# Optimization experiments

Hardware: AMD Instinct MI355X
Metric: run time of the kernel (lower is better)

## Reference

```python
import jax, jax.numpy as jnp
import numpy as np

EMBED_DIM = 1024
N_HEADS = 16
DK = EMBED_DIM // N_HEADS


def setup_inputs() -> dict:
    key = jax.random.key(0)
    ks = jax.random.split(key, 8)
    B, S, D = 2, 2048, EMBED_DIM
    s = 1.0 / np.sqrt(D)
    return {
        'key': jax.random.normal(ks[0], (B, S, D), jnp.float32),
        'query': jax.random.normal(ks[1], (B, S, D), jnp.float32),
        'value': jax.random.normal(ks[2], (B, S, D), jnp.float32),
        'Wq': jax.random.normal(ks[3], (D, D), jnp.float32) * s,
        'Wk': jax.random.normal(ks[4], (D, D), jnp.float32) * s,
        'Wv': jax.random.normal(ks[5], (D, D), jnp.float32) * s,
        'Wo': jax.random.normal(ks[6], (D, D), jnp.float32) * s,
        'bo': jax.random.normal(ks[7], (D,), jnp.float32) * 0.01,
    }


def reference(key, query, value, Wq, Wk, Wv, Wo, bo):
    # torch nn.Linear computes x @ W.T; weights here are [out, in]
    B, Sk, D = key.shape
    Sq = query.shape[1]
    H, dk = N_HEADS, DK
    # project and split heads: [B, H, S, dk]
    Q = (query @ Wq.T).reshape(B, Sq, H, dk).transpose(0, 2, 1, 3)
    K = (key @ Wk.T).reshape(B, Sk, H, dk).transpose(0, 2, 1, 3)
    V = (value @ Wv.T).reshape(B, Sk, H, dk).transpose(0, 2, 1, 3)
    scores = jnp.einsum('bhqd,bhkd->bhqk', Q, K) / jnp.sqrt(jnp.float32(dk))
    attn = jax.nn.softmax(scores, axis=-1)
    ctx = jnp.einsum('bhqk,bhkd->bhqd', attn, V)  # [B, H, Sq, dk]
    concat = ctx.transpose(0, 2, 1, 3).reshape(B, Sq, H * dk)
    return concat @ Wo.T + bo
```

## Files before the change

kernel.cpp:

```cpp
#include <hip/hip_runtime.h>
#include <hip/hip_bf16.h>
#include <stdint.h>


#define D_MODEL 1024
#define NH      16
#define DKH     64
#define SEQ     2048
#define BATCH   2
#define M_TOT   (BATCH * SEQ)
#define XSZ     (M_TOT * D_MODEL)
#define WSZ     (D_MODEL * D_MODEL)
#define NT      (SEQ / 64)
#define NKT     (D_MODEL / 64)

#define SCALE_Q 0.18033688011112042f
#define SHIFT2  5.770780163555854f

typedef _Float16 f16x8 __attribute__((ext_vector_type(8)));
typedef _Float16 f16x4 __attribute__((ext_vector_type(4)));
typedef __fp16   h16x2 __attribute__((ext_vector_type(2)));
typedef float    f32x4v __attribute__((ext_vector_type(4)));

typedef __attribute__((address_space(1))) const void gas_void;
typedef __attribute__((address_space(3))) void las_void;

__device__ __forceinline__ void gload16(const _Float16* g, _Float16* l) {
    __builtin_amdgcn_global_load_lds((gas_void*)g, (las_void*)l, 16, 0, 0);
}

__device__ __forceinline__ float fast_exp2(float x) {
    return __builtin_amdgcn_exp2f(x);
}

__global__ __launch_bounds__(256)
void cvt_all(const float* __restrict__ xq, const float* __restrict__ xk,
             const float* __restrict__ xv,
             const float* __restrict__ wq, const float* __restrict__ wk,
             const float* __restrict__ wv, const float* __restrict__ wo,
             _Float16* __restrict__ oxq, _Float16* __restrict__ oxk,
             _Float16* __restrict__ oxv,
             _Float16* __restrict__ owq, _Float16* __restrict__ owk,
             _Float16* __restrict__ owv, _Float16* __restrict__ owo) {
    const int z = blockIdx.z;
    if (z >= 3 && blockIdx.x >= WSZ / 1024) return;
    const float* s = z == 0 ? xq : z == 1 ? xk : z == 2 ? xv :
                     z == 3 ? wq : z == 4 ? wk : z == 5 ? wv : wo;
    _Float16*    d = z == 0 ? oxq : z == 1 ? oxk : z == 2 ? oxv :
                     z == 3 ? owq : z == 4 ? owk : z == 5 ? owv : owo;
    float sc = z == 3 ? SCALE_Q : 1.0f;
    int i = blockIdx.x * 256 + threadIdx.x;
    float4 x = ((const float4*)s)[i];
    f16x4 h = {(_Float16)(x.x * sc), (_Float16)(x.y * sc),
               (_Float16)(x.z * sc), (_Float16)(x.w * sc)};
    ((f16x4*)d)[i] = h;
}

__global__ __launch_bounds__(256)
void qkv_proj(const _Float16* __restrict__ Xq, const _Float16* __restrict__ Xk,
              const _Float16* __restrict__ Xv,
              const _Float16* __restrict__ Wq, const _Float16* __restrict__ Wk,
              const _Float16* __restrict__ Wv,
              _Float16* __restrict__ Qo, _Float16* __restrict__ Ko,
              _Float16* __restrict__ Vt) {
    const int which = blockIdx.z;
    const _Float16* X = which == 0 ? Xq : which == 1 ? Xk : Xv;
    const _Float16* W = which == 0 ? Wq : which == 1 ? Wk : Wv;

    __shared__ __align__(16) _Float16 A[2 * 128 * 64];
    __shared__ __align__(16) _Float16 B[2 * 64 * 64];

    const int t = threadIdx.x;
    const int lane = t & 63, wv = t >> 6;
    const int l15 = lane & 15, quad = lane >> 4;
    const int wm = (wv >> 1) * 64, wn = (wv & 1) * 32;
    const int n0 = blockIdx.y * 64, m0 = blockIdx.x * 128;
    const int srow = lane >> 3;
    const int scol = ((lane & 7) ^ srow) * 8;

    const int achunk0 = wv * 4;
    const int arow0 = achunk0 * 8 + srow;
    const int aldsb = achunk0 * 512 + lane * 8;
    const int bchunk0 = wv * 2;
    const int brow0 = bchunk0 * 8 + srow;
    const int bldsb = bchunk0 * 512 + lane * 8;

    f32x4v acc[4][2] = {};

    #pragma unroll
    for (int c = 0; c < 4; ++c)
        gload16(X + (size_t)(m0 + arow0 + c * 8) * D_MODEL + scol,
                &A[aldsb + c * 512]);
    #pragma unroll
    for (int c = 0; c < 2; ++c)
        gload16(W + (size_t)(n0 + brow0 + c * 8) * D_MODEL + scol,
                &B[bldsb + c * 512]);

    for (int kt = 0; kt < NKT; ++kt) {
        const int acb = (kt & 1) * 8192, apb = acb ^ 8192;
        const int bcb = (kt & 1) * 4096, bpb = bcb ^ 4096;

        __builtin_amdgcn_s_barrier();

        if (kt < NKT - 1) {
            const int k0 = (kt + 1) * 64;
            #pragma unroll
            for (int c = 0; c < 4; ++c)
                gload16(X + (size_t)(m0 + arow0 + c * 8) * D_MODEL + k0 + scol,
                        &A[apb + aldsb + c * 512]);
            #pragma unroll
            for (int c = 0; c < 2; ++c)
                gload16(W + (size_t)(n0 + brow0 + c * 8) * D_MODEL + k0 + scol,
                        &B[bpb + bldsb + c * 512]);
            asm volatile("s_waitcnt vmcnt(6)" ::: "memory");
        } else {
            asm volatile("s_waitcnt vmcnt(0)" ::: "memory");
        }
        __builtin_amdgcn_sched_barrier(0);

        #pragma unroll
        for (int ks = 0; ks < 2; ++ks) {
            const int g = ((ks * 4 + quad) ^ (l15 & 7)) * 8;
            f16x8 a[4], b[2];
            #pragma unroll
            for (int mi = 0; mi < 4; ++mi)
                a[mi] = *(const f16x8*)&A[acb + (wm + mi * 16 + l15) * 64 + g];
            #pragma unroll
            for (int ni = 0; ni < 2; ++ni)
                b[ni] = *(const f16x8*)&B[bcb + (wn + ni * 16 + l15) * 64 + g];
            #pragma unroll
            for (int mi = 0; mi < 4; ++mi)
                #pragma unroll
                for (int ni = 0; ni < 2; ++ni)
                    acc[mi][ni] = __builtin_amdgcn_mfma_f32_16x16x32_f16(
                        a[mi], b[ni], acc[mi][ni], 0, 0, 0);
        }
    }

    #pragma unroll
    for (int mi = 0; mi < 4; ++mi)
        #pragma unroll
        for (int r = 0; r < 4; ++r) {
            int m = m0 + wm + mi * 16 + quad * 4 + r;
            int bb = m >> 11, s = m & (SEQ - 1);
            #pragma unroll
            for (int ni = 0; ni < 2; ++ni) {
                int col = n0 + wn + ni * 16 + l15;
                int h = col >> 6, d = col & 63;
                _Float16 v = (_Float16)acc[mi][ni][r];
                if (which == 2)
                    Vt[((size_t)(bb * NH + h) * DKH + d) * SEQ + s] = v;
                else if (which == 0)
                    Qo[((size_t)(bb * NH + h) * SEQ + s) * DKH + d] = v;
                else
                    Ko[((size_t)(bb * NH + h) * SEQ + s) * DKH + d] = v;
            }
        }
}

__global__ __launch_bounds__(512)
void attn_kernel(const _Float16* __restrict__ Qg, const _Float16* __restrict__ Kg,
                 const _Float16* __restrict__ Vtg, _Float16* __restrict__ Cg) {
    __shared__ __align__(16) _Float16 Qs[128 * 64];
    __shared__ __align__(16) _Float16 Ks[2 * 64 * 64];
    __shared__ __align__(16) _Float16 Vs[2 * 64 * 64];
    __shared__ __align__(16) _Float16 PsT[128 * 64];
    const int t = threadIdx.x;
    const int lane = t & 63, wv = t >> 6;
    const int l15 = lane & 15, quad = lane >> 4;
    const int bh = blockIdx.x, q0 = blockIdx.y * 128;
    const _Float16* Qb = Qg + (size_t)bh * SEQ * DKH;
    const _Float16* Kb = Kg + (size_t)bh * SEQ * DKH;
    const _Float16* Vb = Vtg + (size_t)bh * DKH * SEQ;

    const int srow = lane >> 3;
    const int scol = ((lane & 7) ^ srow) * 8;
    const int r7 = l15 & 7;

    const int krow = wv * 8 + srow;
    const int off = wv * 512 + lane * 8;
    const _Float16* kp = Kb + (size_t)krow * DKH + scol;
    const _Float16* vp = Vb + (size_t)krow * SEQ + scol;

    #pragma unroll
    for (int c = 0; c < 2; ++c) {
        int chunk = wv * 2 + c;
        int row = chunk * 8 + srow;
        gload16(Qb + (size_t)(q0 + row) * DKH + scol, &Qs[chunk * 512 + lane * 8]);
    }
    gload16(kp, &Ks[off]);
    gload16(vp, &Vs[off]);
    __syncthreads();

    f16x8 bq[2];
    {
        int row = wv * 16 + l15;
        #pragma unroll
        for (int ks = 0; ks < 2; ++ks)
            bq[ks] = *(const f16x8*)&Qs[row * 64 +
                                        (((ks * 4 + quad) ^ (row & 7)) * 8)];
    }

    f32x4v O[4] = {};
    f32x4v lacc = {};
    const f16x8 ones = {(_Float16)1.0f, (_Float16)1.0f, (_Float16)1.0f,
                        (_Float16)1.0f, (_Float16)1.0f, (_Float16)1.0f,
                        (_Float16)1.0f, (_Float16)1.0f};

    const _Float16* kA = kp + 64 * DKH;
    const _Float16* vA = vp + 64;

    for (int ti = 0; ti < NT; ++ti) {
        const int cb = (ti & 1) * 4096;
        const int pb = cb ^ 4096;

        __builtin_amdgcn_s_barrier();

        if (ti < NT - 1) {
            gload16(kA, &Ks[pb + off]);
            gload16(vA, &Vs[pb + off]);
            kA += 64 * DKH; vA += 64;
            asm volatile("s_waitcnt vmcnt(2)" ::: "memory");
        } else {
            asm volatile("s_waitcnt vmcnt(0)" ::: "memory");
        }
        __builtin_amdgcn_sched_barrier(0);

        f32x4v sf[4];
        #pragma unroll
        for (int c = 0; c < 4; ++c)
            sf[c] = f32x4v{-SHIFT2, -SHIFT2, -SHIFT2, -SHIFT2};

        __builtin_amdgcn_s_setprio(1);
        #pragma unroll
        for (int ks = 0; ks < 2; ++ks) {
            const int g = ((ks * 4 + quad) ^ r7) * 8;
            #pragma unroll
            for (int c = 0; c < 4; ++c) {
                f16x8 ak = *(const f16x8*)&Ks[cb + (c * 16 + l15) * 64 + g];
                sf[c] = __builtin_amdgcn_mfma_f32_16x16x32_f16(
                    ak, bq[ks], sf[c], 0, 0, 0);
            }
        }
        __builtin_amdgcn_s_setprio(0);

        const int prow = wv * 16 + l15;
        #pragma unroll
        for (int c = 0; c < 4; ++c) {
            float p0 = fast_exp2(sf[c][0]);
            float p1 = fast_exp2(sf[c][1]);
            float p2 = fast_exp2(sf[c][2]);
            float p3 = fast_exp2(sf[c][3]);
            union { f16x4 v; h16x2 h[2]; } u;
            u.h[0] = __builtin_amdgcn_cvt_pkrtz(p0, p1);
            u.h[1] = __builtin_amdgcn_cvt_pkrtz(p2, p3);
            const int swzcol = (((2 * c + (quad >> 1)) ^ r7) * 8) +
                               (quad & 1) * 4;
            *(f16x4*)&PsT[prow * 64 + swzcol] = u.v;
        }

        #pragma unroll
        for (int ks = 0; ks < 2; ++ks) {
            const int g = ((ks * 4 + quad) ^ r7) * 8;
            f16x8 bp = *(const f16x8*)&PsT[prow * 64 + g];
            __builtin_amdgcn_s_setprio(1);
            lacc = __builtin_amdgcn_mfma_f32_16x16x32_f16(
                ones, bp, lacc, 0, 0, 0);
            #pragma unroll
            for (int di = 0; di < 4; ++di) {
                f16x8 av = *(const f16x8*)&Vs[cb + (di * 16 + l15) * 64 + g];
                O[di] = __builtin_amdgcn_mfma_f32_16x16x32_f16(
                    av, bp, O[di], 0, 0, 0);
            }
            __builtin_amdgcn_s_setprio(0);
        }
    }

    {
        float inv = 1.0f / lacc[0];
        int q = q0 + wv * 16 + l15;
        _Float16* Crow = Cg + ((size_t)bh * SEQ + q) * DKH;
        #pragma unroll
        for (int di = 0; di < 4; ++di) {
            f16x4 oh = {(_Float16)(O[di][0] * inv), (_Float16)(O[di][1] * inv),
                        (_Float16)(O[di][2] * inv), (_Float16)(O[di][3] * inv)};
            *(f16x4*)&Crow[di * 16 + quad * 4] = oh;
        }
    }
}

__global__ __launch_bounds__(256)
void oproj(const _Float16* __restrict__ Ch, const _Float16* __restrict__ Wo,
           const float* __restrict__ bo, float* __restrict__ out) {
    __shared__ __align__(16) _Float16 A[2 * 64 * 64];
    __shared__ __align__(16) _Float16 B[2 * 128 * 64];
    const int t = threadIdx.x;
    const int lane = t & 63, wv = t >> 6;
    const int l15 = lane & 15, quad = lane >> 4;
    const int wm = (wv >> 1) * 32, wn = (wv & 1) * 64;
    const int n0 = blockIdx.y * 128, m0 = blockIdx.x * 64;
    const int srow = lane >> 3;
    const int scol = ((lane & 7) ^ srow) * 8;
    const int bb = m0 >> 11, sbase = m0 & (SEQ - 1);

    const int achunk0 = wv * 2;
    const int arow0 = achunk0 * 8 + srow;
    const int aldsb = achunk0 * 512 + lane * 8;
    const int bchunk0 = wv * 4;
    const int brow0 = bchunk0 * 8 + srow;
    const int bldsb = bchunk0 * 512 + lane * 8;

    f32x4v acc[2][4] = {};

    #pragma unroll
    for (int c = 0; c < 2; ++c)
        gload16(Ch + ((size_t)(bb * NH + 0) * SEQ + sbase + arow0 + c * 8) * DKH + scol,
                &A[aldsb + c * 512]);
    #pragma unroll
    for (int c = 0; c < 4; ++c)
        gload16(Wo + (size_t)(n0 + brow0 + c * 8) * D_MODEL + scol,
                &B[bldsb + c * 512]);

    for (int kt = 0; kt < NKT; ++kt) {
        const int acb = (kt & 1) * 4096, apb = acb ^ 4096;
        const int bcb = (kt & 1) * 8192, bpb = bcb ^ 8192;

        __builtin_amdgcn_s_barrier();

        if (kt < NKT - 1) {
            const int h = kt + 1, k0 = (kt + 1) * 64;
            #pragma unroll
            for (int c = 0; c < 2; ++c)
                gload16(Ch + ((size_t)(bb * NH + h) * SEQ + sbase + arow0 + c * 8) * DKH + scol,
                        &A[apb + aldsb + c * 512]);
            #pragma unroll
            for (int c = 0; c < 4; ++c)
                gload16(Wo + (size_t)(n0 + brow0 + c * 8) * D_MODEL + k0 + scol,
                        &B[bpb + bldsb + c * 512]);
            asm volatile("s_waitcnt vmcnt(6)" ::: "memory");
        } else {
            asm volatile("s_waitcnt vmcnt(0)" ::: "memory");
        }
        __builtin_amdgcn_sched_barrier(0);

        #pragma unroll
        for (int ks = 0; ks < 2; ++ks) {
            const int g = ((ks * 4 + quad) ^ (l15 & 7)) * 8;
            f16x8 a[2], b[4];
            #pragma unroll
            for (int mi = 0; mi < 2; ++mi)
                a[mi] = *(const f16x8*)&A[acb + (wm + mi * 16 + l15) * 64 + g];
            #pragma unroll
            for (int ni = 0; ni < 4; ++ni)
                b[ni] = *(const f16x8*)&B[bcb + (wn + ni * 16 + l15) * 64 + g];
            #pragma unroll
            for (int mi = 0; mi < 2; ++mi)
                #pragma unroll
                for (int ni = 0; ni < 4; ++ni)
                    acc[mi][ni] = __builtin_amdgcn_mfma_f32_16x16x32_f16(
                        a[mi], b[ni], acc[mi][ni], 0, 0, 0);
        }
    }
    #pragma unroll
    for (int ni = 0; ni < 4; ++ni) {
        int col = n0 + wn + ni * 16 + l15;
        float bv = bo[col];
        #pragma unroll
        for (int mi = 0; mi < 2; ++mi)
            #pragma unroll
            for (int r = 0; r < 4; ++r) {
                int row = m0 + wm + mi * 16 + quad * 4 + r;
                out[(size_t)row * D_MODEL + col] = acc[mi][ni][r] + bv;
            }
    }
}

extern "C" void kernel_launch(void* const* d_in, const int* in_sizes, int n_in,
                              void* d_out, int out_size, void* d_ws, size_t ws_size,
                              hipStream_t stream) {
    (void)in_sizes; (void)n_in; (void)out_size; (void)ws_size;
    const float* key   = (const float*)d_in[0];
    const float* query = (const float*)d_in[1];
    const float* value = (const float*)d_in[2];
    const float* Wq    = (const float*)d_in[3];
    const float* Wk    = (const float*)d_in[4];
    const float* Wv    = (const float*)d_in[5];
    const float* Wo    = (const float*)d_in[6];
    const float* bo    = (const float*)d_in[7];
    float* out = (float*)d_out;

    _Float16* w   = (_Float16*)d_ws;
    _Float16* Xq  = w;
    _Float16* Xk  = Xq + XSZ;
    _Float16* Xv  = Xk + XSZ;
    _Float16* Wqh = Xv + XSZ;
    _Float16* Wkh = Wqh + WSZ;
    _Float16* Wvh = Wkh + WSZ;
    _Float16* Woh = Wvh + WSZ;
    _Float16* Qh  = Woh + WSZ;
    _Float16* Kh  = Qh + XSZ;
    _Float16* Vt  = Kh + XSZ;
    _Float16* Chx = Vt + XSZ;

    cvt_all<<<dim3(XSZ / 1024, 1, 7), 256, 0, stream>>>(
        query, key, value, Wq, Wk, Wv, Wo,
        Xq, Xk, Xv, Wqh, Wkh, Wvh, Woh);
    qkv_proj<<<dim3(M_TOT / 128, D_MODEL / 64, 3), 256, 0, stream>>>(
        Xq, Xk, Xv, Wqh, Wkh, Wvh, Qh, Kh, Vt);
    attn_kernel<<<dim3(BATCH * NH, SEQ / 128), 512, 0, stream>>>(Qh, Kh, Vt, Chx);
    oproj<<<dim3(M_TOT / 64, D_MODEL / 128), 256, 0, stream>>>(Chx, Woh, bo, out);
}
```

Before: 210.7 us.

## Switch attention kernel to 32x32x16 MFMA with wave pairs splitting keys

Rewrites the attention inner loop around 32x32x16 MFMA tiles. Pairs of waves now share a 32-query block: each wave computes scores for half of the 64-key tile, writes its exp'd probabilities to shared memory, and then computes half of the head dimension of the output. The larger MFMA shape is meant to cut instruction count and LDS fragment reads per flop. The cost is an extra workgroup barrier per key tile, because waves now read P written by their partner, plus a different accumulator layout.

After: 216.9 us. 2.9% more time.

```diff
diff --git a/kernel.cpp b/kernel.cpp
--- a/kernel.cpp
+++ b/kernel.cpp
@@ -21,6 +21,7 @@
 typedef _Float16 f16x4 __attribute__((ext_vector_type(4)));
 typedef __fp16   h16x2 __attribute__((ext_vector_type(2)));
 typedef float    f32x4v __attribute__((ext_vector_type(4)));
+typedef float    f32x16 __attribute__((ext_vector_type(16)));
 
 typedef __attribute__((address_space(1))) const void gas_void;
 typedef __attribute__((address_space(3))) void las_void;
@@ -167,7 +168,8 @@
     __shared__ __align__(16) _Float16 PsT[128 * 64];
     const int t = threadIdx.x;
     const int lane = t & 63, wv = t >> 6;
-    const int l15 = lane & 15, quad = lane >> 4;
+    const int l31 = lane & 31, h = lane >> 5;
+    const int qb = wv >> 1, kh = wv & 1;
     const int bh = blockIdx.x, q0 = blockIdx.y * 128;
     const _Float16* Qb = Qg + (size_t)bh * SEQ * DKH;
     const _Float16* Kb = Kg + (size_t)bh * SEQ * DKH;
@@ -175,7 +177,6 @@
 
     const int srow = lane >> 3;
     const int scol = ((lane & 7) ^ srow) * 8;
-    const int r7 = l15 & 7;
 
     const int krow = wv * 8 + srow;
     const int off = wv * 512 + lane * 8;
@@ -192,17 +193,18 @@
     gload16(vp, &Vs[off]);
     __syncthreads();
 
-    f16x8 bq[2];
-    {
-        int row = wv * 16 + l15;
-        #pragma unroll
-        for (int ks = 0; ks < 2; ++ks)
-            bq[ks] = *(const f16x8*)&Qs[row * 64 +
-                                        (((ks * 4 + quad) ^ (row & 7)) * 8)];
-    }
-
-    f32x4v O[4] = {};
-    f32x4v lacc = {};
+    const int qrow = qb * 32 + l31;
+    const int q7 = qrow & 7;
+    f16x8 bq[4];
+    #pragma unroll
+    for (int c16 = 0; c16 < 4; ++c16)
+        bq[c16] = *(const f16x8*)&Qs[qrow * 64 + (((c16 * 2 + h) ^ q7) * 8)];
+
+    const int arow = kh * 32 + l31;
+    const int r7a = arow & 7;
+
+    f32x16 O = {};
+    f32x16 lacc = {};
     const f16x8 ones = {(_Float16)1.0f, (_Float16)1.0f, (_Float16)1.0f,
                         (_Float16)1.0f, (_Float16)1.0f, (_Float16)1.0f,
                         (_Float16)1.0f, (_Float16)1.0f};
@@ -226,65 +228,57 @@
         }
         __builtin_amdgcn_sched_barrier(0);
 
-        f32x4v sf[4];
-        #pragma unroll
-        for (int c = 0; c < 4; ++c)
-            sf[c] = f32x4v{-SHIFT2, -SHIFT2, -SHIFT2, -SHIFT2};
+        f32x16 sf;
+        #pragma unroll
+        for (int i = 0; i < 16; ++i) sf[i] = -SHIFT2;
 
         __builtin_amdgcn_s_setprio(1);
         #pragma unroll
-        for (int ks = 0; ks < 2; ++ks) {
-            const int g = ((ks * 4 + quad) ^ r7) * 8;
-            #pragma unroll
-            for (int c = 0; c < 4; ++c) {
-                f16x8 ak = *(const f16x8*)&Ks[cb + (c * 16 + l15) * 64 + g];
-                sf[c] = __builtin_amdgcn_mfma_f32_16x16x32_f16(
-                    ak, bq[ks], sf[c], 0, 0, 0);
-            }
+        for (int c16 = 0; c16 < 4; ++c16) {
+            f16x8 ak = *(const f16x8*)&Ks[cb + arow * 64 +
+                                          (((c16 * 2 + h) ^ r7a) * 8)];
+            sf = __builtin_amdgcn_mfma_f32_32x32x16_f16(ak, bq[c16], sf, 0, 0, 0);
         }
         __builtin_amdgcn_s_setprio(0);
 
-        const int prow = wv * 16 + l15;
-        #pragma unroll
-        for (int c = 0; c < 4; ++c) {
-            float p0 = fast_exp2(sf[c][0]);
-            float p1 = fast_exp2(sf[c][1]);
-            float p2 = fast_exp2(sf[c][2]);
-            float p3 = fast_exp2(sf[c][3]);
-            union { f16x4 v; h16x2 h[2]; } u;
-            u.h[0] = __builtin_amdgcn_cvt_pkrtz(p0, p1);
-            u.h[1] = __builtin_amdgcn_cvt_pkrtz(p2, p3);
-            const int swzcol = (((2 * c + (quad >> 1)) ^ r7) * 8) +
-                               (quad & 1) * 4;
-            *(f16x4*)&PsT[prow * 64 + swzcol] = u.v;
-        }
-
-        #pragma unroll
-        for (int ks = 0; ks < 2; ++ks) {
-            const int g = ((ks * 4 + quad) ^ r7) * 8;
-            f16x8 bp = *(const f16x8*)&PsT[prow * 64 + g];
-            __builtin_amdgcn_s_setprio(1);
-            lacc = __builtin_amdgcn_mfma_f32_16x16x32_f16(
-                ones, bp, lacc, 0, 0, 0);
-            #pragma unroll
-            for (int di = 0; di < 4; ++di) {
-                f16x8 av = *(const f16x8*)&Vs[cb + (di * 16 + l15) * 64 + g];
-                O[di] = __builtin_amdgcn_mfma_f32_16x16x32_f16(
-                    av, bp, O[di], 0, 0, 0);
-            }
-            __builtin_amdgcn_s_setprio(0);
-        }
+        #pragma unroll
+        for (int cl = 0; cl < 4; ++cl) {
+            float p0 = fast_exp2(sf[cl * 4 + 0]);
+            float p1 = fast_exp2(sf[cl * 4 + 1]);
+            float p2 = fast_exp2(sf[cl * 4 + 2]);
+            float p3 = fast_exp2(sf[cl * 4 + 3]);
+            union { f16x4 v; h16x2 hh[2]; } u;
+            u.hh[0] = __builtin_amdgcn_cvt_pkrtz(p0, p1);
+            u.hh[1] = __builtin_amdgcn_cvt_pkrtz(p2, p3);
+            *(f16x4*)&PsT[qrow * 64 + (((kh * 4 + cl) ^ q7) * 8) + h * 4] = u.v;
+        }
+
+        asm volatile("s_waitcnt lgkmcnt(0)" ::: "memory");
+        __builtin_amdgcn_s_barrier();
+
+        __builtin_amdgcn_s_setprio(1);
+        #pragma unroll
+        for (int kc = 0; kc < 4; ++kc) {
+            f16x8 bp = *(const f16x8*)&PsT[qrow * 64 + (((kc * 2 + h) ^ q7) * 8)];
+            lacc = __builtin_amdgcn_mfma_f32_32x32x16_f16(ones, bp, lacc, 0, 0, 0);
+            f16x8 av = *(const f16x8*)&Vs[cb + arow * 64 +
+                                          (((kc * 2 + h) ^ r7a) * 8)];
+            O = __builtin_amdgcn_mfma_f32_32x32x16_f16(av, bp, O, 0, 0, 0);
+        }
+        __builtin_amdgcn_s_setprio(0);
     }
 
     {
         float inv = 1.0f / lacc[0];
-        int q = q0 + wv * 16 + l15;
+        int q = q0 + qrow;
         _Float16* Crow = Cg + ((size_t)bh * SEQ + q) * DKH;
         #pragma unroll
-        for (int di = 0; di < 4; ++di) {
-            f16x4 oh = {(_Float16)(O[di][0] * inv), (_Float16)(O[di][1] * inv),
-                        (_Float16)(O[di][2] * inv), (_Float16)(O[di][3] * inv)};
-            *(f16x4*)&Crow[di * 16 + quad * 4] = oh;
+        for (int cl = 0; cl < 4; ++cl) {
+            f16x4 oh = {(_Float16)(O[cl * 4 + 0] * inv),
+                        (_Float16)(O[cl * 4 + 1] * inv),
+                        (_Float16)(O[cl * 4 + 2] * inv),
+                        (_Float16)(O[cl * 4 + 3] * inv)};
+            *(f16x4*)&Crow[kh * 32 + cl * 8 + h * 4] = oh;
         }
     }
 }
```
